# Kernel optimization log

Measured on AMD Instinct MI355X. Metric: run time of the kernel, lower is better.

Reference implementation:

```python
import jax, jax.numpy as jnp
import numpy as np

N = 50000      # nodes
E = 800000     # edges
IN = 64        # in_channels
HID = 128      # hidden_channels
HEADS = 4
D = HID // HEADS  # 32 per-head dim
G = 64         # graphs in batch


def setup_inputs() -> dict:
    key = jax.random.key(0)
    ks = jax.random.split(key, 24)
    def p(k, shape):
        return (jax.random.normal(k, shape, jnp.float32) * 0.05)
    x = jax.random.normal(ks[0], (N, IN), jnp.float32)
    edge_index = jax.random.randint(ks[1], (2, E), 0, N, dtype=jnp.int32).astype(jnp.int64)
    batch = jnp.sort(jax.random.randint(ks[2], (N,), 0, G, dtype=jnp.int32)).astype(jnp.int64)
    inp = {"x": x, "edge_index": edge_index, "batch": batch}
    # layer 1: in -> HID (heads*D), with root/skip projection
    inp["Wq1"] = p(ks[3], (IN, HID)); inp["bq1"] = p(ks[4], (HID,))
    inp["Wk1"] = p(ks[5], (IN, HID)); inp["bk1"] = p(ks[6], (HID,))
    inp["Wv1"] = p(ks[7], (IN, HID)); inp["bv1"] = p(ks[8], (HID,))
    inp["Ws1"] = p(ks[9], (IN, HID)); inp["bs1"] = p(ks[10], (HID,))
    # layer 2: HID -> HID
    inp["Wq2"] = p(ks[11], (HID, HID)); inp["bq2"] = p(ks[12], (HID,))
    inp["Wk2"] = p(ks[13], (HID, HID)); inp["bk2"] = p(ks[14], (HID,))
    inp["Wv2"] = p(ks[15], (HID, HID)); inp["bv2"] = p(ks[16], (HID,))
    inp["Ws2"] = p(ks[17], (HID, HID)); inp["bs2"] = p(ks[18], (HID,))
    # readout linear HID -> 2
    inp["Wl"] = p(ks[19], (HID, 2)); inp["bl"] = p(ks[20], (2,))
    return inp


def transformer_conv(x, src, dst, Wq, bq, Wk, bk, Wv, bv, Ws, bs):
    """PyG TransformerConv (concat=True, root_weight=True, beta=False, eval mode)."""
    n = x.shape[0]
    q = (x @ Wq + bq).reshape(n, HEADS, D)
    k = (x @ Wk + bk).reshape(n, HEADS, D)
    v = (x @ Wv + bv).reshape(n, HEADS, D)
    # per-edge attention logits: query at target (dst), key/value at source (src)
    qi, kj, vj = q[dst], k[src], v[src]           # [E, H, D]
    logits = jnp.sum(qi * kj, axis=-1) / jnp.sqrt(jnp.asarray(D, x.dtype))  # [E, H]
    # segment softmax over incoming edges of each target node
    m = jax.ops.segment_max(logits, dst, num_segments=n)   # [N, H]
    p = jnp.exp(logits - m[dst])                           # [E, H]
    s = jax.ops.segment_sum(p, dst, num_segments=n)        # [N, H]
    alpha = p / s[dst]                                     # [E, H]
    agg = jax.ops.segment_sum(alpha[..., None] * vj, dst, num_segments=n)  # [N, H, D]
    out = agg.reshape(n, HID) + (x @ Ws + bs)              # concat heads + skip
    return out


def reference(x, edge_index, batch,
              Wq1, bq1, Wk1, bk1, Wv1, bv1, Ws1, bs1,
              Wq2, bq2, Wk2, bk2, Wv2, bv2, Ws2, bs2,
              Wl, bl):
    src, dst = edge_index[0], edge_index[1]
    h = jax.nn.relu(transformer_conv(x, src, dst, Wq1, bq1, Wk1, bk1, Wv1, bv1, Ws1, bs1))
    h = jax.nn.relu(transformer_conv(h, src, dst, Wq2, bq2, Wk2, bk2, Wv2, bv2, Ws2, bs2))
    # global mean pool per graph
    counts = jax.ops.segment_sum(jnp.ones((h.shape[0],), h.dtype), batch, num_segments=G)
    pooled = jax.ops.segment_sum(h, batch, num_segments=G) / jnp.maximum(counts, 1.0)[:, None]
    return pooled @ Wl + bl  # [G, 2]
```

## Files before the change

kernel.cpp:

```cpp
#include <hip/hip_runtime.h>
#include <hip/hip_bf16.h>
#include <cstdint>
#include <cstddef>

#define N_NODES 50000
#define N_EDGES 800000
#define IN_CH 64
#define HID_CH 128
#define N_GRAPHS 64

#define NB_SCAN ((N_NODES + 255) / 256)
#define NB_CNT4 ((N_EDGES + 1023) / 1024)
#define NB_GEMM ((N_NODES + 63) / 64)
#define NB_GEMM4 (NB_GEMM * 4)
#define W_ELEMS (4 * IN_CH * 128 + 4 * HID_CH * 128)
#define NB_CONV ((W_ELEMS + 255) / 256)

typedef short s16x8 __attribute__((ext_vector_type(8)));
typedef float f32x4 __attribute__((ext_vector_type(4)));
typedef float f32x2 __attribute__((ext_vector_type(2)));

__device__ __forceinline__ float bf2f(__hip_bfloat16 v) { return __bfloat162float(v); }
__device__ __forceinline__ float bfbits2f(unsigned hs) {
  union { unsigned u; float f; } v; v.u = hs << 16; return v.f;
}
__device__ __forceinline__ float bfhi2f(unsigned w) {
  union { unsigned u; float f; } v; v.u = w & 0xffff0000u; return v.f;
}
__device__ __forceinline__ short f2bfs(float f) {
  __hip_bfloat16 h = __float2bfloat16(f); return *(short*)&h;
}
__device__ __forceinline__ unsigned short f2bfu(float f) {
  __hip_bfloat16 h = __float2bfloat16(f); return *(unsigned short*)&h;
}
__device__ __forceinline__ int clamp_id(int v) {
  if (v < 0) v = 0;
  if (v >= N_NODES) v = N_NODES - 1;
  return v;
}

__device__ __forceinline__ unsigned char f2fp8(float v) {
  return (unsigned char)(__builtin_amdgcn_cvt_pk_fp8_f32(v, v, 0, false) & 0xff);
}
template<bool HI>
__device__ __forceinline__ f32x2 fp8pair(unsigned w) {
  return __builtin_amdgcn_cvt_pk_f32_fp8(w, HI);
}

__global__ __launch_bounds__(256)
void prep(const int* __restrict__ ei, int* __restrict__ cnt,
          unsigned short* __restrict__ rank,
          const float* __restrict__ w1q, const float* __restrict__ w1k,
          const float* __restrict__ w1v, const float* __restrict__ w1s,
          const float* __restrict__ w2q, const float* __restrict__ w2k,
          const float* __restrict__ w2v, const float* __restrict__ w2s,
          __hip_bfloat16* d1q, __hip_bfloat16* d1k, __hip_bfloat16* d1v, __hip_bfloat16* d1s,
          __hip_bfloat16* d2q, __hip_bfloat16* d2k, __hip_bfloat16* d2v, __hip_bfloat16* d2s)
{
  int bx = blockIdx.x;
  if (bx < NB_CNT4) {
    int e0 = bx * 1024 + threadIdx.x * 4;
    if (e0 >= N_EDGES) return;
    if (e0 + 3 < N_EDGES) {
      int4 dv = *(const int4*)(ei + N_EDGES + e0);
      unsigned short r0 = (unsigned short)atomicAdd(&cnt[clamp_id(dv.x)], 1);
      unsigned short r1 = (unsigned short)atomicAdd(&cnt[clamp_id(dv.y)], 1);
      unsigned short r2 = (unsigned short)atomicAdd(&cnt[clamp_id(dv.z)], 1);
      unsigned short r3 = (unsigned short)atomicAdd(&cnt[clamp_id(dv.w)], 1);
      ushort4 rv; rv.x = r0; rv.y = r1; rv.z = r2; rv.w = r3;
      *(ushort4*)(rank + e0) = rv;
    } else {
      for (int j = 0; j < 4; ++j)
        if (e0 + j < N_EDGES)
          rank[e0 + j] = (unsigned short)atomicAdd(&cnt[clamp_id(ei[N_EDGES + e0 + j])], 1);
    }
    return;
  }
  int j = (bx - NB_CNT4) * 256 + threadIdx.x;
  if (j >= W_ELEMS) return;
  const float* S[8] = {w1q, w1k, w1v, w1s, w2q, w2k, w2v, w2s};
  __hip_bfloat16* D[8] = {d1q, d1k, d1v, d1s, d2q, d2k, d2v, d2s};
  int m, r;
  if (j < 4 * IN_CH * 128) { m = j >> 13; r = j & 8191; }
  else { int jj = j - 4 * IN_CH * 128; m = 4 + (jj >> 14); r = jj & 16383; }
  int k = r >> 7, c = r & 127;
  D[m][(((k >> 3) * 128 + c) << 3) + (k & 7)] = __float2bfloat16(S[m][r]);
}

template<int KD, int XF32>
__device__ __forceinline__ void gemm_body_onemat(
    int bg, int mat, const void* X,
    const short* __restrict__ WT, const float* __restrict__ bias,
    short* Qo, unsigned char* KV8, short* So, short* lds)
{
  constexpr int KT = KD / 32;
  constexpr int CHUNKS = KD * 16;
  const int tid  = threadIdx.x;
  const int wid  = tid >> 6;
  const int lane = tid & 63;
  const int quad = lane >> 4;
  const int mm   = lane & 15;
  const int rt   = wid & 1;
  const int ch   = wid >> 1;
  const int rowbase = bg * 64 + rt * 32;

  {
    const uint4* src = (const uint4*)WT;
    uint4* dst = (uint4*)lds;
    #pragma unroll
    for (int i = 0; i < CHUNKS / 256; ++i)
      dst[tid + i * 256] = src[tid + i * 256];
  }

  s16x8 afrag[2][KT];
  #pragma unroll
  for (int t = 0; t < 2; ++t) {
    const int arow = rowbase + t * 16 + mm;
    if (arow < N_NODES) {
      if (XF32) {
        const float* xp = (const float*)X + (size_t)arow * KD;
        #pragma unroll
        for (int kt = 0; kt < KT; ++kt) {
          const float4* p = (const float4*)(xp + kt * 32 + quad * 8);
          float4 a = p[0], b = p[1];
          s16x8 fr;
          fr[0] = f2bfs(a.x); fr[1] = f2bfs(a.y); fr[2] = f2bfs(a.z); fr[3] = f2bfs(a.w);
          fr[4] = f2bfs(b.x); fr[5] = f2bfs(b.y); fr[6] = f2bfs(b.z); fr[7] = f2bfs(b.w);
          afrag[t][kt] = fr;
        }
      } else {
        const short* xp = (const short*)X + (size_t)arow * KD;
        #pragma unroll
        for (int kt = 0; kt < KT; ++kt)
          afrag[t][kt] = *(const s16x8*)(xp + kt * 32 + quad * 8);
      }
    } else {
      #pragma unroll
      for (int kt = 0; kt < KT; ++kt)
        afrag[t][kt] = (s16x8){0,0,0,0,0,0,0,0};
    }
  }

  __syncthreads();

  f32x4 acc[4][2];
  #pragma unroll
  for (int c4 = 0; c4 < 4; ++c4) {
    float b = bias[ch * 64 + c4 * 16 + mm];
    f32x4 av = {b, b, b, b};
    acc[c4][0] = av; acc[c4][1] = av;
  }
  #pragma unroll
  for (int kt = 0; kt < KT; ++kt) {
    #pragma unroll
    for (int c4 = 0; c4 < 4; ++c4) {
      s16x8 bfrag = *(const s16x8*)(lds + ((((kt * 4 + quad) << 7) + ch * 64 + c4 * 16 + mm) << 3));
      acc[c4][0] = __builtin_amdgcn_mfma_f32_16x16x32_bf16(afrag[0][kt], bfrag, acc[c4][0], 0, 0, 0);
      acc[c4][1] = __builtin_amdgcn_mfma_f32_16x16x32_bf16(afrag[1][kt], bfrag, acc[c4][1], 0, 0, 0);
    }
  }

  if (mat == 1 || mat == 2) {
    unsigned char* O8 = KV8 + ((mat == 1) ? 0 : 128);
    #pragma unroll
    for (int c4 = 0; c4 < 4; ++c4) {
      const int col = ch * 64 + c4 * 16 + mm;
      #pragma unroll
      for (int t = 0; t < 2; ++t) {
        #pragma unroll
        for (int r = 0; r < 4; ++r) {
          int row = rowbase + t * 16 + quad * 4 + r;
          if (row < N_NODES)
            O8[(size_t)row * 256 + col] = f2fp8(acc[c4][t][r]);
        }
      }
    }
  } else {
    short* O = (mat == 0) ? Qo : So;
    #pragma unroll
    for (int c4 = 0; c4 < 4; ++c4) {
      const int col = ch * 64 + c4 * 16 + mm;
      #pragma unroll
      for (int t = 0; t < 2; ++t) {
        #pragma unroll
        for (int r = 0; r < 4; ++r) {
          int row = rowbase + t * 16 + quad * 4 + r;
          if (row < N_NODES)
            ((__hip_bfloat16*)O)[(size_t)row * 128 + col] = __float2bfloat16(acc[c4][t][r]);
        }
      }
    }
  }
}

__global__ __launch_bounds__(256)
void scan1(const int* __restrict__ cnt, int* __restrict__ offs, int* __restrict__ bsum) {
  __shared__ int wsum[4];
  int t = threadIdx.x, lane = t & 63, w = t >> 6;
  int i = blockIdx.x * 256 + t;
  int v = (i < N_NODES) ? cnt[i] : 0;
  int x = v;
  #pragma unroll
  for (int o = 1; o < 64; o <<= 1) { int y = __shfl_up(x, o, 64); if (lane >= o) x += y; }
  if (lane == 63) wsum[w] = x;
  __syncthreads();
  if (t == 0) {
    int run = 0;
    #pragma unroll
    for (int k = 0; k < 4; ++k) { int tv = wsum[k]; wsum[k] = run; run += tv; }
    bsum[blockIdx.x] = run;
  }
  __syncthreads();
  if (i <= N_NODES) offs[i] = wsum[w] + x - v;
}

__global__ __launch_bounds__(256)
void scan2(int* __restrict__ bsum) {
  __shared__ int wsum[4];
  int t = threadIdx.x, lane = t & 63, w = t >> 6;
  int v = (t < NB_SCAN) ? bsum[t] : 0;
  int x = v;
  #pragma unroll
  for (int o = 1; o < 64; o <<= 1) { int y = __shfl_up(x, o, 64); if (lane >= o) x += y; }
  if (lane == 63) wsum[w] = x;
  __syncthreads();
  if (t == 0) {
    int run = 0;
    #pragma unroll
    for (int k = 0; k < 4; ++k) { int tv = wsum[k]; wsum[k] = run; run += tv; }
  }
  __syncthreads();
  if (t < NB_SCAN) bsum[t] = wsum[w] + x - v;
}

__global__ __launch_bounds__(256)
void scatter_gemm1(const int* __restrict__ ei, const int* __restrict__ offs,
                   const int* __restrict__ bsum, const unsigned short* __restrict__ rank,
                   int* __restrict__ ssrc,
                   const float* __restrict__ X,
                   const short* __restrict__ w1q, const short* __restrict__ w1k,
                   const short* __restrict__ w1v, const short* __restrict__ w1s,
                   const float* __restrict__ b1q, const float* __restrict__ b1k,
                   const float* __restrict__ b1v, const float* __restrict__ b1s,
                   short* Qb, unsigned char* KV8, short* Sb)
{
  __shared__ short lds[IN_CH * 128];
  int bx = blockIdx.x;
  if (bx >= NB_GEMM4) {
    int e0 = (bx - NB_GEMM4) * 1024 + threadIdx.x * 4;
    if (e0 >= N_EDGES) return;
    if (e0 + 3 < N_EDGES) {
      int4 sv = *(const int4*)(ei + e0);
      int4 dv = *(const int4*)(ei + N_EDGES + e0);
      ushort4 rv = *(const ushort4*)(rank + e0);
      int d0 = clamp_id(dv.x), d1 = clamp_id(dv.y);
      int d2 = clamp_id(dv.z), d3 = clamp_id(dv.w);
      int p0 = offs[d0] + bsum[d0 >> 8] + rv.x;
      int p1 = offs[d1] + bsum[d1 >> 8] + rv.y;
      int p2 = offs[d2] + bsum[d2 >> 8] + rv.z;
      int p3 = offs[d3] + bsum[d3 >> 8] + rv.w;
      ssrc[p0] = clamp_id(sv.x);
      ssrc[p1] = clamp_id(sv.y);
      ssrc[p2] = clamp_id(sv.z);
      ssrc[p3] = clamp_id(sv.w);
    } else {
      for (int j = 0; j < 4; ++j) {
        int e = e0 + j;
        if (e < N_EDGES) {
          int src = clamp_id(ei[e]);
          int dst = clamp_id(ei[N_EDGES + e]);
          ssrc[offs[dst] + bsum[dst >> 8] + rank[e]] = src;
        }
      }
    }
    return;
  }
  const int bg  = bx >> 2;
  const int mat = bx & 3;
  const short* wts[4] = {w1q, w1k, w1v, w1s};
  const float* bias[4] = {b1q, b1k, b1v, b1s};
  gemm_body_onemat<IN_CH, 1>(bg, mat, X, wts[mat], bias[mat], Qb, KV8, Sb, lds);
}

__global__ __launch_bounds__(256)
void attn_kernel(const unsigned short* __restrict__ Q, const unsigned char* __restrict__ KV8,
                 const unsigned short* S,
                 const int* __restrict__ offs, const int* __restrict__ bsum,
                 const int* __restrict__ ssrc, unsigned short* H)
{
  const int dst = blockIdx.x * 4 + (threadIdx.x >> 6);
  if (dst >= N_NODES) return;
  const int lane = threadIdx.x & 63;
  const int sub  = lane >> 4;
  const int cl   = lane & 15;

  const float qs = 0.17677669529663687f * 1.4426950408889634f;
  uint4 qw = *(const uint4*)(Q + (size_t)dst * 128 + cl * 8);
  float q[8], a[8];
  #pragma unroll
  for (int i = 0; i < 4; ++i) {
    unsigned w = ((unsigned*)&qw)[i];
    q[2 * i]     = bfbits2f(w & 0xffffu) * qs;
    q[2 * i + 1] = bfhi2f(w) * qs;
    a[2 * i] = 0.f; a[2 * i + 1] = 0.f;
  }
  float s = 0.f;

  const int e0 = offs[dst] + bsum[dst >> 8];
  const int e1 = offs[dst + 1] + bsum[(dst + 1) >> 8];
  const int iters = (e1 - e0 + 3) >> 2;

  if (iters > 0) {
    int e = e0 + sub;
    bool have = (e < e1);
    int src = have ? ssrc[e] : ssrc[e0];
    float ph = have ? 1.f : 0.f;
    const unsigned char* kvp = KV8 + (size_t)src * 256 + cl * 8;
    uint2 kw = *(const uint2*)(kvp);
    uint2 vw = *(const uint2*)(kvp + 128);

    for (int it = 0; it < iters; ++it) {
      uint2 kwn, vwn;
      int en = e + 4;
      bool haven = (en < e1);
      float phn = haven ? 1.f : 0.f;
      if (it + 1 < iters) {
        int srcn = haven ? ssrc[en] : ssrc[e0];
        const unsigned char* kvn = KV8 + (size_t)srcn * 256 + cl * 8;
        kwn = *(const uint2*)(kvn);
        vwn = *(const uint2*)(kvn + 128);
      } else {
        kwn = kw; vwn = vw;
      }
      f32x2 k0 = fp8pair<false>(kw.x), k1 = fp8pair<true>(kw.x);
      f32x2 k2 = fp8pair<false>(kw.y), k3 = fp8pair<true>(kw.y);
      float d = q[0] * k0.x + q[1] * k0.y + q[2] * k1.x + q[3] * k1.y
              + q[4] * k2.x + q[5] * k2.y + q[6] * k3.x + q[7] * k3.y;
      d += __shfl_xor(d, 1, 64);
      d += __shfl_xor(d, 2, 64);
      float p = exp2f(d) * ph;
      s += p;
      f32x2 v0 = fp8pair<false>(vw.x), v1 = fp8pair<true>(vw.x);
      f32x2 v2 = fp8pair<false>(vw.y), v3 = fp8pair<true>(vw.y);
      a[0] += p * v0.x; a[1] += p * v0.y;
      a[2] += p * v1.x; a[3] += p * v1.y;
      a[4] += p * v2.x; a[5] += p * v2.y;
      a[6] += p * v3.x; a[7] += p * v3.y;
      kw = kwn; vw = vwn; ph = phn; e = en;
    }
  }

  s += __shfl_xor(s, 16, 64);
  s += __shfl_xor(s, 32, 64);
  #pragma unroll
  for (int i = 0; i < 8; ++i) {
    a[i] += __shfl_xor(a[i], 16, 64);
    a[i] += __shfl_xor(a[i], 32, 64);
  }
  const float inv = (s > 0.f) ? (1.0f / s) : 0.f;

  if (sub == 0) {
    uint4 sw = *(const uint4*)(S + (size_t)dst * 128 + cl * 8);
    uint4 ow;
    #pragma unroll
    for (int i = 0; i < 4; ++i) {
      unsigned w = ((unsigned*)&sw)[i];
      float o0 = fmaxf(a[2 * i] * inv     + bfbits2f(w & 0xffffu), 0.f);
      float o1 = fmaxf(a[2 * i + 1] * inv + bfhi2f(w), 0.f);
      ((unsigned*)&ow)[i] = (unsigned)f2bfu(o0) | ((unsigned)f2bfu(o1) << 16);
    }
    *(uint4*)(H + (size_t)dst * 128 + cl * 8) = ow;
  }
}

__global__ __launch_bounds__(256)
void gemm2(const short* __restrict__ X,
           const short* __restrict__ w2q, const short* __restrict__ w2k,
           const short* __restrict__ w2v, const short* __restrict__ w2s,
           const float* __restrict__ b2q, const float* __restrict__ b2k,
           const float* __restrict__ b2v, const float* __restrict__ b2s,
           short* Qb, unsigned char* KV8, short* Sb2)
{
  __shared__ short lds[HID_CH * 128];
  const int bg  = blockIdx.x >> 2;
  const int mat = blockIdx.x & 3;
  const short* wts[4] = {w2q, w2k, w2v, w2s};
  const float* bias[4] = {b2q, b2k, b2v, b2s};
  gemm_body_onemat<HID_CH, 0>(bg, mat, X, wts[mat], bias[mat], Qb, KV8, Sb2, lds);
}

__device__ __forceinline__ int lower_bound_i(const int* __restrict__ b, int n, int val) {
  int lo = 0, hi = n;
  while (lo < hi) { int mid = (lo + hi) >> 1; if (b[mid] < val) lo = mid + 1; else hi = mid; }
  return lo;
}

__global__ __launch_bounds__(128)
void pool_partial(const __hip_bfloat16* __restrict__ H, const int* __restrict__ batch,
                  float* __restrict__ pooled)
{
  const int g = blockIdx.x >> 4, p = blockIdx.x & 15, t = threadIdx.x;
  const int s = lower_bound_i(batch, N_NODES, g);
  const int e = lower_bound_i(batch, N_NODES, g + 1);
  const int len = e - s;
  if (len <= 0) return;
  const int chunk = (len + 15) >> 4;
  const int a = s + p * chunk;
  const int b = min(a + chunk, e);
  if (a >= b) return;
  float sum = 0.f;
  for (int i = a; i < b; ++i) sum += bf2f(H[(size_t)i * 128 + t]);
  atomicAdd(&pooled[g * 128 + t], sum);
}

__global__ __launch_bounds__(128)
void pool_final(const float* __restrict__ pooled, const int* __restrict__ batch,
                const float* __restrict__ Wl, const float* __restrict__ bl,
                float* __restrict__ out)
{
  const int g = blockIdx.x, t = threadIdx.x;
  __shared__ float r0[128], r1[128];
  const int s = lower_bound_i(batch, N_NODES, g);
  const int e = lower_bound_i(batch, N_NODES, g + 1);
  const float inv = 1.0f / (float)max(e - s, 1);
  const float pc = pooled[g * 128 + t] * inv;
  r0[t] = pc * Wl[t * 2 + 0];
  r1[t] = pc * Wl[t * 2 + 1];
  __syncthreads();
  for (int o = 64; o > 0; o >>= 1) {
    if (t < o) { r0[t] += r0[t + o]; r1[t] += r1[t + o]; }
    __syncthreads();
  }
  if (t == 0) {
    out[g * 2 + 0] = r0[0] + bl[0];
    out[g * 2 + 1] = r1[0] + bl[1];
  }
}


extern "C" void kernel_launch(void* const* d_in, const int* in_sizes, int n_in,
                              void* d_out, int out_size, void* d_ws, size_t ws_size,
                              hipStream_t stream) {
  uintptr_t base = (uintptr_t)d_ws;
  auto take = [&](size_t bytes) -> uintptr_t {
    uintptr_t p = base;
    base += (bytes + 255) & ~(size_t)255;
    return p;
  };

  int*   cnt    = (int*)take((size_t)N_NODES * 4);
  float* pooled = (float*)take((size_t)N_GRAPHS * 128 * 4);
  int*   offs   = (int*)take((size_t)(N_NODES + 1) * 4);
  int*   bsum   = (int*)take((size_t)NB_SCAN * 4);
  int*   ssrc   = (int*)take((size_t)N_EDGES * 4);
  unsigned short* rank = (unsigned short*)take((size_t)N_EDGES * 2);
  short* Qb     = (short*)take((size_t)N_NODES * 128 * 2);
  unsigned char* KV8 = (unsigned char*)take((size_t)N_NODES * 256);
  short* Sb     = (short*)take((size_t)N_NODES * 128 * 2);
  short* Sb2    = (short*)take((size_t)N_NODES * 128 * 2);
  short* wt1q   = (short*)take((size_t)IN_CH * 128 * 2);
  short* wt1k   = (short*)take((size_t)IN_CH * 128 * 2);
  short* wt1v   = (short*)take((size_t)IN_CH * 128 * 2);
  short* wt1s   = (short*)take((size_t)IN_CH * 128 * 2);
  short* wt2q   = (short*)take((size_t)HID_CH * 128 * 2);
  short* wt2k   = (short*)take((size_t)HID_CH * 128 * 2);
  short* wt2v   = (short*)take((size_t)HID_CH * 128 * 2);
  short* wt2s   = (short*)take((size_t)HID_CH * 128 * 2);

  const int* ei    = (const int*)d_in[1];
  const int* batch = (const int*)d_in[2];

  size_t zspan = (size_t)((char*)pooled + (size_t)N_GRAPHS * 128 * 4 - (char*)cnt);
  hipMemsetAsync(cnt, 0, zspan, stream);

  prep<<<NB_CNT4 + NB_CONV, 256, 0, stream>>>(
      ei, cnt, rank,
      (const float*)d_in[3], (const float*)d_in[5], (const float*)d_in[7], (const float*)d_in[9],
      (const float*)d_in[11], (const float*)d_in[13], (const float*)d_in[15], (const float*)d_in[17],
      (__hip_bfloat16*)wt1q, (__hip_bfloat16*)wt1k, (__hip_bfloat16*)wt1v, (__hip_bfloat16*)wt1s,
      (__hip_bfloat16*)wt2q, (__hip_bfloat16*)wt2k, (__hip_bfloat16*)wt2v, (__hip_bfloat16*)wt2s);

  scan1<<<NB_SCAN, 256, 0, stream>>>(cnt, offs, bsum);
  scan2<<<1, 256, 0, stream>>>(bsum);

  scatter_gemm1<<<NB_GEMM4 + NB_CNT4, 256, 0, stream>>>(
      ei, offs, bsum, rank, ssrc,
      (const float*)d_in[0],
      wt1q, wt1k, wt1v, wt1s,
      (const float*)d_in[4], (const float*)d_in[6], (const float*)d_in[8], (const float*)d_in[10],
      Qb, KV8, Sb);

  const int attn_grid = (N_NODES + 3) / 4;

  attn_kernel<<<attn_grid, 256, 0, stream>>>(
      (const unsigned short*)Qb, KV8,
      (const unsigned short*)Sb, offs, bsum, ssrc, (unsigned short*)Sb);

  gemm2<<<NB_GEMM4, 256, 0, stream>>>(
      Sb, wt2q, wt2k, wt2v, wt2s,
      (const float*)d_in[12], (const float*)d_in[14], (const float*)d_in[16], (const float*)d_in[18],
      Qb, KV8, Sb2);

  attn_kernel<<<attn_grid, 256, 0, stream>>>(
      (const unsigned short*)Qb, KV8,
      (const unsigned short*)Sb2, offs, bsum, ssrc, (unsigned short*)Sb2);

  pool_partial<<<N_GRAPHS * 16, 128, 0, stream>>>(
      (const __hip_bfloat16*)Sb2, batch, pooled);
  pool_final<<<N_GRAPHS, 128, 0, stream>>>(pooled, batch, (const float*)d_in[19],
                                           (const float*)d_in[20], (float*)d_out);
}
```

Baseline: 305.9 us.

## Loop GEMM blocks over multiple row tiles with prefetched A fragments

Each GEMM block now handles four 64-row tiles instead of one. The LDS weight tile is loaded once per block and reused across them, and the A fragments for the next tile are loaded into registers while the current tile's MFMAs run. The scatter blocks are also moved ahead of the GEMM blocks in the fused launch. This cuts repeated weight loads and block launch overhead, at the cost of four times fewer blocks (less parallelism) and higher register pressure from double-buffered fragments.

```diff
diff --git a/kernel.cpp b/kernel.cpp
--- a/kernel.cpp
+++ b/kernel.cpp
@@ -11,8 +11,9 @@
 
 #define NB_SCAN ((N_NODES + 255) / 256)
 #define NB_CNT4 ((N_EDGES + 1023) / 1024)
-#define NB_GEMM ((N_NODES + 63) / 64)
-#define NB_GEMM4 (NB_GEMM * 4)
+#define ROWG 4
+#define NB_GRP ((N_NODES + 64 * ROWG - 1) / (64 * ROWG))
+#define NB_GEMM_L (NB_GRP * 4)
 #define W_ELEMS (4 * IN_CH * 128 + 4 * HID_CH * 128)
 #define NB_CONV ((W_ELEMS + 255) / 256)
 
@@ -88,8 +89,8 @@
 }
 
 template<int KD, int XF32>
-__device__ __forceinline__ void gemm_body_onemat(
-    int bg, int mat, const void* X,
+__device__ __forceinline__ void gemm_body_loop(
+    int grp, int mat, const void* X,
     const short* __restrict__ WT, const float* __restrict__ bias,
     short* Qo, unsigned char* KV8, short* So, short* lds)
 {
@@ -102,7 +103,6 @@
   const int mm   = lane & 15;
   const int rt   = wid & 1;
   const int ch   = wid >> 1;
-  const int rowbase = bg * 64 + rt * 32;
 
   {
     const uint4* src = (const uint4*)WT;
@@ -112,84 +112,108 @@
       dst[tid + i * 256] = src[tid + i * 256];
   }
 
-  s16x8 afrag[2][KT];
+  float bv[4];
   #pragma unroll
-  for (int t = 0; t < 2; ++t) {
-    const int arow = rowbase + t * 16 + mm;
-    if (arow < N_NODES) {
-      if (XF32) {
-        const float* xp = (const float*)X + (size_t)arow * KD;
-        #pragma unroll
-        for (int kt = 0; kt < KT; ++kt) {
-          const float4* p = (const float4*)(xp + kt * 32 + quad * 8);
-          float4 a = p[0], b = p[1];
-          s16x8 fr;
-          fr[0] = f2bfs(a.x); fr[1] = f2bfs(a.y); fr[2] = f2bfs(a.z); fr[3] = f2bfs(a.w);
-          fr[4] = f2bfs(b.x); fr[5] = f2bfs(b.y); fr[6] = f2bfs(b.z); fr[7] = f2bfs(b.w);
-          afrag[t][kt] = fr;
+  for (int c4 = 0; c4 < 4; ++c4) bv[c4] = bias[ch * 64 + c4 * 16 + mm];
+
+  auto loadA = [&](int bg, s16x8 fr[2][KT]) {
+    const int rowbase = bg * 64 + rt * 32;
+    #pragma unroll
+    for (int t = 0; t < 2; ++t) {
+      const int arow = rowbase + t * 16 + mm;
+      if (arow < N_NODES) {
+        if (XF32) {
+          const float* xp = (const float*)X + (size_t)arow * KD;
+          #pragma unroll
+          for (int kt = 0; kt < KT; ++kt) {
+            const float4* p = (const float4*)(xp + kt * 32 + quad * 8);
+            float4 a = p[0], b = p[1];
+            s16x8 f;
+            f[0] = f2bfs(a.x); f[1] = f2bfs(a.y); f[2] = f2bfs(a.z); f[3] = f2bfs(a.w);
+            f[4] = f2bfs(b.x); f[5] = f2bfs(b.y); f[6] = f2bfs(b.z); f[7] = f2bfs(b.w);
+            fr[t][kt] = f;
+          }
+        } else {
+          const short* xp = (const short*)X + (size_t)arow * KD;
+          #pragma unroll
+          for (int kt = 0; kt < KT; ++kt)
+            fr[t][kt] = *(const s16x8*)(xp + kt * 32 + quad * 8);
         }
       } else {
-        const short* xp = (const short*)X + (size_t)arow * KD;
         #pragma unroll
         for (int kt = 0; kt < KT; ++kt)
-          afrag[t][kt] = *(const s16x8*)(xp + kt * 32 + quad * 8);
+          fr[t][kt] = (s16x8){0,0,0,0,0,0,0,0};
       }
-    } else {
+    }
+  };
+
+  __syncthreads();
+
+  const int bg0 = grp * ROWG;
+  s16x8 cur[2][KT], nxt[2][KT];
+  loadA(bg0, cur);
+
+  #pragma unroll
+  for (int g = 0; g < ROWG; ++g) {
+    const int bg = bg0 + g;
+    const bool act = (bg * 64 < N_NODES);
+    if (g + 1 < ROWG) loadA(bg0 + g + 1, nxt);
+
+    if (act) {
+      const int rowbase = bg * 64 + rt * 32;
+      f32x4 acc[4][2];
       #pragma unroll
-      for (int kt = 0; kt < KT; ++kt)
-        afrag[t][kt] = (s16x8){0,0,0,0,0,0,0,0};
-    }
-  }
-
-  __syncthreads();
-
-  f32x4 acc[4][2];
-  #pragma unroll
-  for (int c4 = 0; c4 < 4; ++c4) {
-    float b = bias[ch * 64 + c4 * 16 + mm];
-    f32x4 av = {b, b, b, b};
-    acc[c4][0] = av; acc[c4][1] = av;
-  }
-  #pragma unroll
-  for (int kt = 0; kt < KT; ++kt) {
-    #pragma unroll
-    for (int c4 = 0; c4 < 4; ++c4) {
-      s16x8 bfrag = *(const s16x8*)(lds + ((((kt * 4 + quad) << 7) + ch * 64 + c4 * 16 + mm) << 3));
-      acc[c4][0] = __builtin_amdgcn_mfma_f32_16x16x32_bf16(afrag[0][kt], bfrag, acc[c4][0], 0, 0, 0);
-      acc[c4][1] = __builtin_amdgcn_mfma_f32_16x16x32_bf16(afrag[1][kt], bfrag, acc[c4][1], 0, 0, 0);
-    }
-  }
-
-  if (mat == 1 || mat == 2) {
-    unsigned char* O8 = KV8 + ((mat == 1) ? 0 : 128);
-    #pragma unroll
-    for (int c4 = 0; c4 < 4; ++c4) {
-      const int col = ch * 64 + c4 * 16 + mm;
+      for (int c4 = 0; c4 < 4; ++c4) {
+        f32x4 av = {bv[c4], bv[c4], bv[c4], bv[c4]};
+        acc[c4][0] = av; acc[c4][1] = av;
+      }
       #pragma unroll
-      for (int t = 0; t < 2; ++t) {
+      for (int kt = 0; kt < KT; ++kt) {
         #pragma unroll
-        for (int r = 0; r < 4; ++r) {
-          int row = rowbase + t * 16 + quad * 4 + r;
-          if (row < N_NODES)
-            O8[(size_t)row * 256 + col] = f2fp8(acc[c4][t][r]);
+        for (int c4 = 0; c4 < 4; ++c4) {
+          s16x8 bfrag = *(const s16x8*)(lds + ((((kt * 4 + quad) << 7) + ch * 64 + c4 * 16 + mm) << 3));
+          acc[c4][0] = __builtin_amdgcn_mfma_f32_16x16x32_bf16(cur[0][kt], bfrag, acc[c4][0], 0, 0, 0);
+          acc[c4][1] = __builtin_amdgcn_mfma_f32_16x16x32_bf16(cur[1][kt], bfrag, acc[c4][1], 0, 0, 0);
+        }
+      }
+      if (mat == 1 || mat == 2) {
+        unsigned char* O8 = KV8 + ((mat == 1) ? 0 : 128);
+        #pragma unroll
+        for (int c4 = 0; c4 < 4; ++c4) {
+          const int col = ch * 64 + c4 * 16 + mm;
+          #pragma unroll
+          for (int t = 0; t < 2; ++t) {
+            #pragma unroll
+            for (int r = 0; r < 4; ++r) {
+              int row = rowbase + t * 16 + quad * 4 + r;
+              if (row < N_NODES)
+                O8[(size_t)row * 256 + col] = f2fp8(acc[c4][t][r]);
+            }
+          }
+        }
+      } else {
+        short* O = (mat == 0) ? Qo : So;
+        #pragma unroll
+        for (int c4 = 0; c4 < 4; ++c4) {
+          const int col = ch * 64 + c4 * 16 + mm;
+          #pragma unroll
+          for (int t = 0; t < 2; ++t) {
+            #pragma unroll
+            for (int r = 0; r < 4; ++r) {
+              int row = rowbase + t * 16 + quad * 4 + r;
+              if (row < N_NODES)
+                ((__hip_bfloat16*)O)[(size_t)row * 128 + col] = __float2bfloat16(acc[c4][t][r]);
+            }
+          }
         }
       }
     }
-  } else {
-    short* O = (mat == 0) ? Qo : So;
+
     #pragma unroll
-    for (int c4 = 0; c4 < 4; ++c4) {
-      const int col = ch * 64 + c4 * 16 + mm;
+    for (int t = 0; t < 2; ++t)
       #pragma unroll
-      for (int t = 0; t < 2; ++t) {
-        #pragma unroll
-        for (int r = 0; r < 4; ++r) {
-          int row = rowbase + t * 16 + quad * 4 + r;
-          if (row < N_NODES)
-            ((__hip_bfloat16*)O)[(size_t)row * 128 + col] = __float2bfloat16(acc[c4][t][r]);
-        }
-      }
-    }
+      for (int kt = 0; kt < KT; ++kt)
+        cur[t][kt] = nxt[t][kt];
   }
 }
 
@@ -246,8 +270,8 @@
 {
   __shared__ short lds[IN_CH * 128];
   int bx = blockIdx.x;
-  if (bx >= NB_GEMM4) {
-    int e0 = (bx - NB_GEMM4) * 1024 + threadIdx.x * 4;
+  if (bx < NB_CNT4) {
+    int e0 = bx * 1024 + threadIdx.x * 4;
     if (e0 >= N_EDGES) return;
     if (e0 + 3 < N_EDGES) {
       int4 sv = *(const int4*)(ei + e0);
@@ -275,11 +299,12 @@
     }
     return;
   }
-  const int bg  = bx >> 2;
-  const int mat = bx & 3;
+  const int b   = bx - NB_CNT4;
+  const int grp = b >> 2;
+  const int mat = b & 3;
   const short* wts[4] = {w1q, w1k, w1v, w1s};
   const float* bias[4] = {b1q, b1k, b1v, b1s};
-  gemm_body_onemat<IN_CH, 1>(bg, mat, X, wts[mat], bias[mat], Qb, KV8, Sb, lds);
+  gemm_body_loop<IN_CH, 1>(grp, mat, X, wts[mat], bias[mat], Qb, KV8, Sb, lds);
 }
 
 __global__ __launch_bounds__(256)
@@ -382,11 +407,11 @@
            short* Qb, unsigned char* KV8, short* Sb2)
 {
   __shared__ short lds[HID_CH * 128];
-  const int bg  = blockIdx.x >> 2;
+  const int grp = blockIdx.x >> 2;
   const int mat = blockIdx.x & 3;
   const short* wts[4] = {w2q, w2k, w2v, w2s};
   const float* bias[4] = {b2q, b2k, b2v, b2s};
-  gemm_body_onemat<HID_CH, 0>(bg, mat, X, wts[mat], bias[mat], Qb, KV8, Sb2, lds);
+  gemm_body_loop<HID_CH, 0>(grp, mat, X, wts[mat], bias[mat], Qb, KV8, Sb2, lds);
 }
 
 __device__ __forceinline__ int lower_bound_i(const int* __restrict__ b, int n, int val) {
@@ -483,7 +508,7 @@
   scan1<<<NB_SCAN, 256, 0, stream>>>(cnt, offs, bsum);
   scan2<<<1, 256, 0, stream>>>(bsum);
 
-  scatter_gemm1<<<NB_GEMM4 + NB_CNT4, 256, 0, stream>>>(
+  scatter_gemm1<<<NB_CNT4 + NB_GEMM_L, 256, 0, stream>>>(
       ei, offs, bsum, rank, ssrc,
       (const float*)d_in[0],
       wt1q, wt1k, wt1v, wt1s,
@@ -496,7 +521,7 @@
       (const unsigned short*)Qb, KV8,
       (const unsigned short*)Sb, offs, bsum, ssrc, (unsigned short*)Sb);
 
-  gemm2<<<NB_GEMM4, 256, 0, stream>>>(
+  gemm2<<<NB_GEMM_L, 256, 0, stream>>>(
       Sb, wt2q, wt2k, wt2v, wt2s,
       (const float*)d_in[12], (const float*)d_in[14], (const float*)d_in[16], (const float*)d_in[18],
       Qb, KV8, Sb2);
```

Measured after the change: 309.0 us. About the same (+1.0%).
